# Kernel optimization log

Hardware: AMD Instinct MI355X
Metric: run time of the kernel (lower is better)

The kernel has to match this reference:

```python
import jax, jax.numpy as jnp
import numpy as np

NUM_NODES = 200000
NUM_EDGES = 600000
NUM_GRAPHS = 10000
BN_EPS = 1e-5


def setup_inputs() -> dict:
    key = jax.random.key(0)
    ks = jax.random.split(key, 10)
    x = jax.random.normal(ks[0], (NUM_NODES, 78), dtype=jnp.float32)
    edge_index = jax.random.randint(ks[1], (2, NUM_EDGES), 0, NUM_NODES, dtype=jnp.int64 if jax.config.jax_enable_x64 else jnp.int32)
    batch = jnp.sort(jax.random.randint(ks[2], (NUM_NODES,), 0, NUM_GRAPHS))
    def glorot(k, shape):
        fan_in, fan_out = shape[-2], shape[-1]
        s = jnp.sqrt(2.0 / (fan_in + fan_out))
        return jax.random.normal(k, shape, dtype=jnp.float32) * s
    return {
        "x": x,
        "edge_index": edge_index,
        "batch": batch,
        "W1_0": glorot(ks[3], (78, 128)),
        "b1_0": jnp.zeros((128,), jnp.float32),
        "W2_0": glorot(ks[4], (128, 128)),
        "b2_0": jnp.zeros((128,), jnp.float32),
        "g_0": jnp.ones((128,), jnp.float32),
        "be_0": jnp.zeros((128,), jnp.float32),
        "W1s": glorot(ks[5], (4, 128, 128)),
        "b1s": jnp.zeros((4, 128), jnp.float32),
        "W2s": glorot(ks[6], (4, 128, 128)),
        "b2s": jnp.zeros((4, 128), jnp.float32),
        "gs": jnp.ones((4, 128), jnp.float32),
        "bes": jnp.zeros((4, 128), jnp.float32),
        "fcW": glorot(ks[7], (128, 64)),
        "fcb": jnp.zeros((64,), jnp.float32),
    }


def _batchnorm(h, gamma, beta):
    # BatchNorm1d with batch statistics (training-mode normalization)
    mean = h.mean(axis=0)
    var = h.var(axis=0)  # biased, as torch uses for normalization
    return gamma * (h - mean) * jax.lax.rsqrt(var + BN_EPS) + beta


def _gin_block(h, src, dst, W1, b1, W2, b2, gamma, beta):
    # GINConv (eps=0): MLP(x + sum of neighbor messages), then ReLU + BN
    agg = jax.ops.segment_sum(h[src], dst, num_segments=NUM_NODES)  # [N, d]
    z = h + agg
    z = jax.nn.relu(z @ W1 + b1) @ W2 + b2
    z = jax.nn.relu(z)
    return _batchnorm(z, gamma, beta)


def reference(x, edge_index, batch, W1_0, b1_0, W2_0, b2_0, g_0, be_0,
              W1s, b1s, W2s, b2s, gs, bes, fcW, fcb):
    src, dst = edge_index[0], edge_index[1]
    h = _gin_block(x, src, dst, W1_0, b1_0, W2_0, b2_0, g_0, be_0)  # [N, 128]

    def body(h, params):
        W1, b1, W2, b2, g, be = params
        return _gin_block(h, src, dst, W1, b1, W2, b2, g, be), None

    h, _ = jax.lax.scan(body, h, (W1s, b1s, W2s, b2s, gs, bes))

    pooled = jax.ops.segment_sum(h, batch, num_segments=NUM_GRAPHS)  # [G, 128]
    out = jax.nn.relu(pooled @ fcW + fcb)  # [G, 64]; dropout is identity at eval
    return out
```

## Files before the change

kernel.cpp:

```cpp
#include <hip/hip_runtime.h>
#include <hip/hip_bf16.h>

#define NN 200000
#define NE 600000
#define NG 10000
#define NCH 98
#define NTILE 3125

typedef __attribute__((ext_vector_type(8))) short bfrag;
typedef __attribute__((ext_vector_type(4))) float f32x4;
typedef unsigned short u16;

static __device__ __forceinline__ u16 f2b(float x) {
  __hip_bfloat16 b = __float2bfloat16(x);
  return __builtin_bit_cast(u16, b);
}
static __device__ __forceinline__ float b2f(u16 u) {
  __hip_bfloat16 b = __builtin_bit_cast(__hip_bfloat16, u);
  return __bfloat162float(b);
}
static __device__ __forceinline__ void split(float v, u16& hi, u16& lo) {
  hi = f2b(v);
  lo = f2b(v - b2f(hi));
}

__global__ void prep_kernel(const float* __restrict__ W1_0, const float* __restrict__ W2_0,
                            const float* __restrict__ W1s, const float* __restrict__ W2s,
                            u16* __restrict__ wf) {
  int i = blockIdx.x * 256 + threadIdx.x;
  if (i >= 312 * 64) return;
  int t = i >> 6, lane = i & 63;
  const float* W;
  int KS, ct, kk, Krows, base, half;
  if (t < 24) {
    W = W1_0; KS = 3; ct = t / 3; kk = t - ct * 3; Krows = 78; base = 0; half = 12288;
  } else if (t < 56) {
    int u = t - 24;
    W = W2_0; KS = 4; ct = u >> 2; kk = u & 3; Krows = 128; base = 24576; half = 16384;
  } else {
    int u = t - 56;
    int j = u >> 6, r = u & 63;
    KS = 4; Krows = 128; half = 16384;
    if (r < 32) {
      W = W1s + j * 16384; ct = r >> 2; kk = r & 3; base = 57344 + j * 65536;
    } else {
      W = W2s + j * 16384; r -= 32; ct = r >> 2; kk = r & 3; base = 57344 + j * 65536 + 32768;
    }
  }
  int col = ct * 16 + (lane & 15);
  int idx = ((ct * KS + kk) * 64 + lane) * 8;
  for (int jj = 0; jj < 8; jj++) {
    int k = kk * 32 + 8 * (lane >> 4) + jj;
    float v = (k < Krows) ? W[k * 128 + col] : 0.f;
    u16 hi, lo;
    split(v, hi, lo);
    wf[base + idx + jj] = hi;
    wf[base + half + idx + jj] = lo;
  }
}

__global__ void hist_kernel(const int* __restrict__ dst, int* __restrict__ deg) {
  int e = blockIdx.x * 256 + threadIdx.x;
  if (e < NE) atomicAdd(&deg[dst[e]], 1);
}

__global__ void scan1_kernel(const int* __restrict__ deg, int* __restrict__ csum) {
  __shared__ int s[256];
  int base = blockIdx.x * 2048 + threadIdx.x * 8;
  int t = 0;
#pragma unroll
  for (int j = 0; j < 8; j++) {
    int idx = base + j;
    if (idx < NN) t += deg[idx];
  }
  s[threadIdx.x] = t;
  __syncthreads();
  for (int o = 128; o > 0; o >>= 1) {
    if (threadIdx.x < o) s[threadIdx.x] += s[threadIdx.x + o];
    __syncthreads();
  }
  if (threadIdx.x == 0) csum[blockIdx.x] = s[0];
}

__global__ void scan2_kernel(int* __restrict__ csum, int* __restrict__ rowptr) {
  int acc = 0;
  for (int i = 0; i < NCH; i++) {
    int v = csum[i];
    csum[i] = acc;
    acc += v;
  }
  rowptr[NN] = acc;
}

__global__ void scan3_kernel(const int* deg, const int* __restrict__ csum,
                             int* __restrict__ rowptr, int* cursor) {
  __shared__ int s[256];
  int tid = threadIdx.x;
  int base = blockIdx.x * 2048 + tid * 8;
  int loc[8];
  int t = 0;
#pragma unroll
  for (int j = 0; j < 8; j++) {
    int idx = base + j;
    int d = (idx < NN) ? deg[idx] : 0;
    loc[j] = t;
    t += d;
  }
  s[tid] = t;
  __syncthreads();
  for (int o = 1; o < 256; o <<= 1) {
    int u = (tid >= o) ? s[tid - o] : 0;
    __syncthreads();
    s[tid] += u;
    __syncthreads();
  }
  int off = csum[blockIdx.x] + s[tid] - t;
#pragma unroll
  for (int j = 0; j < 8; j++) {
    int idx = base + j;
    if (idx < NN) {
      int r = off + loc[j];
      rowptr[idx] = r;
      cursor[idx] = r;
    }
  }
}

__global__ void scatter_kernel(const int* __restrict__ src, const int* __restrict__ dst,
                               int* __restrict__ cursor, int* __restrict__ csr_src) {
  int e = blockIdx.x * 256 + threadIdx.x;
  if (e < NE) {
    int p = atomicAdd(&cursor[dst[e]], 1);
    csr_src[p] = src[e];
  }
}

template <bool FIRST>
__global__ __launch_bounds__(512, 4) void fused_kernel(
    const float* __restrict__ xin, const u16* __restrict__ hin,
    const float* __restrict__ ss,
    const int* __restrict__ rowptr, const int* __restrict__ csr_src,
    const u16* __restrict__ w1hi, const u16* __restrict__ w1lo,
    const u16* __restrict__ w2hi, const u16* __restrict__ w2lo,
    const float* __restrict__ b1, const float* __restrict__ b2,
    u16* __restrict__ hout, float* __restrict__ stats) {
  constexpr int KS1 = FIRST ? 3 : 4;
  constexpr int AH = 0, AL = 8704, TH = 17408, TL = 26112;
  __shared__ u16 lds[34816];
  const int tid = threadIdx.x;
  const int w = tid >> 6, l = tid & 63;
  const int l15 = l & 15, lg = l >> 4;
  const float bb1 = b1[w * 16 + l15];
  const float bb2 = b2[w * 16 + l15];
  float s_acc = 0.f, q_acc = 0.f;

  if (FIRST) {
    const float2* x2 = reinterpret_cast<const float2*>(xin);
    for (int tile = blockIdx.x; tile < NTILE; tile += gridDim.x) {
      const int rows0 = tile * 64;
      for (int j = 0; j < 8; j++) {
        int row = w * 8 + j;
        int node = rows0 + row;
        int beg = rowptr[node], end = rowptr[node + 1];
        int f0 = l * 2;
        if (f0 < 78) {
          size_t fv = (size_t)(f0 >> 1);
          float2 acc = x2[(size_t)node * 39 + fv];
          for (int i = beg; i < end; i += 4) {
            int last = end - 1;
            int i1 = min(i + 1, last), i2 = min(i + 2, last), i3 = min(i + 3, last);
            int s0 = csr_src[i], s1 = csr_src[i1], s2 = csr_src[i2], s3 = csr_src[i3];
            float2 v0 = x2[(size_t)s0 * 39 + fv];
            float2 v1 = x2[(size_t)s1 * 39 + fv];
            float2 v2 = x2[(size_t)s2 * 39 + fv];
            float2 v3 = x2[(size_t)s3 * 39 + fv];
            int rem = end - i;
            float m1 = rem > 1 ? 1.f : 0.f, m2 = rem > 2 ? 1.f : 0.f, m3 = rem > 3 ? 1.f : 0.f;
            acc.x += v0.x + m1 * v1.x + m2 * v2.x + m3 * v3.x;
            acc.y += v0.y + m1 * v1.y + m2 * v2.y + m3 * v3.y;
          }
          ushort2 oh, ol;
          split(acc.x, oh.x, ol.x);
          split(acc.y, oh.y, ol.y);
          *reinterpret_cast<ushort2*>(&lds[AH + row * 136 + f0]) = oh;
          *reinterpret_cast<ushort2*>(&lds[AL + row * 136 + f0]) = ol;
        } else if (f0 < 96) {
          ushort2 z = {0, 0};
          *reinterpret_cast<ushort2*>(&lds[AH + row * 136 + f0]) = z;
          *reinterpret_cast<ushort2*>(&lds[AL + row * 136 + f0]) = z;
        }
      }
      bfrag w1h[KS1], w1l[KS1];
#pragma unroll
      for (int kk = 0; kk < KS1; kk++) {
        int fi = ((w * KS1 + kk) * 64 + l) * 8;
        w1h[kk] = *reinterpret_cast<const bfrag*>(&w1hi[fi]);
        w1l[kk] = *reinterpret_cast<const bfrag*>(&w1lo[fi]);
      }
      __syncthreads();
#pragma unroll
      for (int rt = 0; rt < 4; rt++) {
        f32x4 acc = {bb1, bb1, bb1, bb1};
        const int arow = (rt * 16 + l15) * 136 + 8 * lg;
#pragma unroll
        for (int kk = 0; kk < KS1; kk++) {
          bfrag ah = *reinterpret_cast<const bfrag*>(&lds[AH + arow + kk * 32]);
          bfrag al = *reinterpret_cast<const bfrag*>(&lds[AL + arow + kk * 32]);
          acc = __builtin_amdgcn_mfma_f32_16x16x32_bf16(al, w1h[kk], acc, 0, 0, 0);
          acc = __builtin_amdgcn_mfma_f32_16x16x32_bf16(ah, w1l[kk], acc, 0, 0, 0);
          acc = __builtin_amdgcn_mfma_f32_16x16x32_bf16(ah, w1h[kk], acc, 0, 0, 0);
        }
#pragma unroll
        for (int r = 0; r < 4; r++) {
          float v = fmaxf(acc[r], 0.f);
          u16 hi, lo;
          split(v, hi, lo);
          int off = (rt * 16 + 4 * lg + r) * 136 + w * 16 + l15;
          lds[TH + off] = hi;
          lds[TL + off] = lo;
        }
      }
      bfrag w2h[4], w2l[4];
#pragma unroll
      for (int kk = 0; kk < 4; kk++) {
        int fi = ((w * 4 + kk) * 64 + l) * 8;
        w2h[kk] = *reinterpret_cast<const bfrag*>(&w2hi[fi]);
        w2l[kk] = *reinterpret_cast<const bfrag*>(&w2lo[fi]);
      }
      __syncthreads();
      u16 o16[16];
#pragma unroll
      for (int rt = 0; rt < 4; rt++) {
        f32x4 acc = {bb2, bb2, bb2, bb2};
        const int arow = (rt * 16 + l15) * 136 + 8 * lg;
#pragma unroll
        for (int kk = 0; kk < 4; kk++) {
          bfrag th = *reinterpret_cast<const bfrag*>(&lds[TH + arow + kk * 32]);
          bfrag tl = *reinterpret_cast<const bfrag*>(&lds[TL + arow + kk * 32]);
          acc = __builtin_amdgcn_mfma_f32_16x16x32_bf16(tl, w2h[kk], acc, 0, 0, 0);
          acc = __builtin_amdgcn_mfma_f32_16x16x32_bf16(th, w2l[kk], acc, 0, 0, 0);
          acc = __builtin_amdgcn_mfma_f32_16x16x32_bf16(th, w2h[kk], acc, 0, 0, 0);
        }
#pragma unroll
        for (int r = 0; r < 4; r++) {
          float v = fmaxf(acc[r], 0.f);
          s_acc += v;
          q_acc += v * v;
          o16[rt * 4 + r] = f2b(v);
        }
      }
      __syncthreads();
#pragma unroll
      for (int rt = 0; rt < 4; rt++)
#pragma unroll
        for (int r = 0; r < 4; r++)
          lds[TH + (rt * 16 + 4 * lg + r) * 136 + w * 16 + l15] = o16[rt * 4 + r];
      __syncthreads();
#pragma unroll
      for (int p2 = 0; p2 < 2; p2++) {
        int row = p2 * 32 + (tid >> 4);
        int c8 = tid & 15;
        bfrag vv = *reinterpret_cast<const bfrag*>(&lds[TH + row * 136 + c8 * 8]);
        *reinterpret_cast<bfrag*>(&hout[(size_t)(rows0 + row) * 128 + c8 * 8]) = vv;
      }
      __syncthreads();
    }
  } else {
    const bfrag* hp = reinterpret_cast<const bfrag*>(hin);
    const int k8v = l15;
    const int k8 = l15 * 8;
    float sc8[8], sh8[8];
#pragma unroll
    for (int j = 0; j < 8; j++) {
      sc8[j] = ss[k8 + j];
      sh8[j] = ss[128 + k8 + j];
    }

    int tile0 = blockIdx.x;
#pragma unroll
    for (int p = 0; p < 2; p++) {
      int row = w * 8 + p * 4 + lg;
      int node = tile0 * 64 + row;
      int beg = rowptr[node], end = rowptr[node + 1];
      float a[8];
      bfrag vs = hp[(size_t)node * 16 + k8v];
#pragma unroll
      for (int j = 0; j < 8; j++) a[j] = b2f((u16)vs[j]);
      for (int i = beg; i < end; i += 4) {
        int last = end - 1;
        int i1 = min(i + 1, last), i2 = min(i + 2, last), i3 = min(i + 3, last);
        int s0 = csr_src[i], s1 = csr_src[i1], s2 = csr_src[i2], s3 = csr_src[i3];
        bfrag v0 = hp[(size_t)s0 * 16 + k8v];
        bfrag v1 = hp[(size_t)s1 * 16 + k8v];
        bfrag v2 = hp[(size_t)s2 * 16 + k8v];
        bfrag v3 = hp[(size_t)s3 * 16 + k8v];
        int rem = end - i;
        float m1 = rem > 1 ? 1.f : 0.f, m2 = rem > 2 ? 1.f : 0.f, m3 = rem > 3 ? 1.f : 0.f;
#pragma unroll
        for (int j = 0; j < 8; j++)
          a[j] += (b2f((u16)v0[j]) + m1 * b2f((u16)v1[j])) +
                  (m2 * b2f((u16)v2[j]) + m3 * b2f((u16)v3[j]));
      }
      float cnt = (float)(end - beg + 1);
      bfrag oh, ol;
#pragma unroll
      for (int j = 0; j < 8; j++) {
        float t = a[j] * sc8[j] + cnt * sh8[j];
        u16 hi, lo;
        split(t, hi, lo);
        oh[j] = (short)hi;
        ol[j] = (short)lo;
      }
      *reinterpret_cast<bfrag*>(&lds[AH + row * 136 + k8]) = oh;
      *reinterpret_cast<bfrag*>(&lds[AL + row * 136 + k8]) = ol;
    }
    __syncthreads();

    for (int tile = tile0; tile < NTILE; tile += gridDim.x) {
      const int rows0 = tile * 64;
      int tn = tile + gridDim.x;
      bool np = tn < NTILE;
      int tnc = np ? tn : tile;

      int begN[2], endN[2];
#pragma unroll
      for (int p = 0; p < 2; p++) {
        int nodeN = tnc * 64 + w * 8 + p * 4 + lg;
        begN[p] = rowptr[nodeN];
        endN[p] = rowptr[nodeN + 1];
      }

      bfrag w1h[4], w1l[4];
#pragma unroll
      for (int kk = 0; kk < 4; kk++) {
        int fi = ((w * 4 + kk) * 64 + l) * 8;
        w1h[kk] = *reinterpret_cast<const bfrag*>(&w1hi[fi]);
        w1l[kk] = *reinterpret_cast<const bfrag*>(&w1lo[fi]);
      }
      f32x4 t1[4];
#pragma unroll
      for (int rt = 0; rt < 4; rt++) {
        f32x4 acc = {bb1, bb1, bb1, bb1};
        const int arow = (rt * 16 + l15) * 136 + 8 * lg;
#pragma unroll
        for (int kk = 0; kk < 4; kk++) {
          bfrag ah = *reinterpret_cast<const bfrag*>(&lds[AH + arow + kk * 32]);
          bfrag al = *reinterpret_cast<const bfrag*>(&lds[AL + arow + kk * 32]);
          acc = __builtin_amdgcn_mfma_f32_16x16x32_bf16(al, w1h[kk], acc, 0, 0, 0);
          acc = __builtin_amdgcn_mfma_f32_16x16x32_bf16(ah, w1l[kk], acc, 0, 0, 0);
          acc = __builtin_amdgcn_mfma_f32_16x16x32_bf16(ah, w1h[kk], acc, 0, 0, 0);
        }
        t1[rt] = acc;
      }
      __syncthreads();

      int s0[2], s1[2], s2[2], s3[2];
      float m0[2], m1[2], m2[2], m3[2], cntN[2];
#pragma unroll
      for (int p = 0; p < 2; p++) {
        int beg = begN[p], end = endN[p];
        int deg = end - beg;
        int last = end - 1;
        int i0 = beg, i1 = min(beg + 1, last), i2 = min(beg + 2, last), i3 = min(beg + 3, last);
        if (deg <= 0) { i0 = 0; i1 = 0; i2 = 0; i3 = 0; }
        s0[p] = csr_src[i0];
        s1[p] = csr_src[i1];
        s2[p] = csr_src[i2];
        s3[p] = csr_src[i3];
        m0[p] = deg > 0 ? 1.f : 0.f;
        m1[p] = deg > 1 ? 1.f : 0.f;
        m2[p] = deg > 2 ? 1.f : 0.f;
        m3[p] = deg > 3 ? 1.f : 0.f;
        cntN[p] = (float)(deg + 1);
      }

#pragma unroll
      for (int rt = 0; rt < 4; rt++) {
#pragma unroll
        for (int r = 0; r < 4; r++) {
          float v = fmaxf(t1[rt][r], 0.f);
          u16 hi, lo;
          split(v, hi, lo);
          int off = (rt * 16 + 4 * lg + r) * 136 + w * 16 + l15;
          lds[TH + off] = hi;
          lds[TL + off] = lo;
        }
      }
      bfrag w2h[4], w2l[4];
#pragma unroll
      for (int kk = 0; kk < 4; kk++) {
        int fi = ((w * 4 + kk) * 64 + l) * 8;
        w2h[kk] = *reinterpret_cast<const bfrag*>(&w2hi[fi]);
        w2l[kk] = *reinterpret_cast<const bfrag*>(&w2lo[fi]);
      }
      __syncthreads();

      bfrag selfN[2], nb0[2], nb1[2], nb2[2], nb3[2];
#pragma unroll
      for (int p = 0; p < 2; p++) {
        int nodeN = tnc * 64 + w * 8 + p * 4 + lg;
        selfN[p] = hp[(size_t)nodeN * 16 + k8v];
        nb0[p] = hp[(size_t)s0[p] * 16 + k8v];
        nb1[p] = hp[(size_t)s1[p] * 16 + k8v];
        nb2[p] = hp[(size_t)s2[p] * 16 + k8v];
        nb3[p] = hp[(size_t)s3[p] * 16 + k8v];
      }

      u16 o16[16];
#pragma unroll
      for (int rt = 0; rt < 4; rt++) {
        f32x4 acc = {bb2, bb2, bb2, bb2};
        const int arow = (rt * 16 + l15) * 136 + 8 * lg;
#pragma unroll
        for (int kk = 0; kk < 4; kk++) {
          bfrag th = *reinterpret_cast<const bfrag*>(&lds[TH + arow + kk * 32]);
          bfrag tl = *reinterpret_cast<const bfrag*>(&lds[TL + arow + kk * 32]);
          acc = __builtin_amdgcn_mfma_f32_16x16x32_bf16(tl, w2h[kk], acc, 0, 0, 0);
          acc = __builtin_amdgcn_mfma_f32_16x16x32_bf16(th, w2l[kk], acc, 0, 0, 0);
          acc = __builtin_amdgcn_mfma_f32_16x16x32_bf16(th, w2h[kk], acc, 0, 0, 0);
        }
#pragma unroll
        for (int r = 0; r < 4; r++) {
          float v = fmaxf(acc[r], 0.f);
          s_acc += v;
          q_acc += v * v;
          o16[rt * 4 + r] = f2b(v);
        }
      }
      __syncthreads();

      if (np) {
#pragma unroll
        for (int p = 0; p < 2; p++) {
          int row = w * 8 + p * 4 + lg;
          float a[8];
#pragma unroll
          for (int j = 0; j < 8; j++) a[j] = b2f((u16)selfN[p][j]);
#pragma unroll
          for (int j = 0; j < 8; j++)
            a[j] += (m0[p] * b2f((u16)nb0[p][j]) + m1[p] * b2f((u16)nb1[p][j])) +
                    (m2[p] * b2f((u16)nb2[p][j]) + m3[p] * b2f((u16)nb3[p][j]));
          int beg = begN[p], end = endN[p];
          for (int i = beg + 4; i < end; i += 4) {
            int last = end - 1;
            int i1 = min(i + 1, last), i2 = min(i + 2, last), i3 = min(i + 3, last);
            int t0 = csr_src[i], t1i = csr_src[i1], t2 = csr_src[i2], t3 = csr_src[i3];
            bfrag v0 = hp[(size_t)t0 * 16 + k8v];
            bfrag v1 = hp[(size_t)t1i * 16 + k8v];
            bfrag v2 = hp[(size_t)t2 * 16 + k8v];
            bfrag v3 = hp[(size_t)t3 * 16 + k8v];
            int rem = end - i;
            float n1 = rem > 1 ? 1.f : 0.f, n2 = rem > 2 ? 1.f : 0.f, n3 = rem > 3 ? 1.f : 0.f;
#pragma unroll
            for (int j = 0; j < 8; j++)
              a[j] += (b2f((u16)v0[j]) + n1 * b2f((u16)v1[j])) +
                      (n2 * b2f((u16)v2[j]) + n3 * b2f((u16)v3[j]));
          }
          bfrag oh, ol;
#pragma unroll
          for (int j = 0; j < 8; j++) {
            float t = a[j] * sc8[j] + cntN[p] * sh8[j];
            u16 hi, lo;
            split(t, hi, lo);
            oh[j] = (short)hi;
            ol[j] = (short)lo;
          }
          *reinterpret_cast<bfrag*>(&lds[AH + row * 136 + k8]) = oh;
          *reinterpret_cast<bfrag*>(&lds[AL + row * 136 + k8]) = ol;
        }
      }

#pragma unroll
      for (int rt = 0; rt < 4; rt++)
#pragma unroll
        for (int r = 0; r < 4; r++)
          lds[TH + (rt * 16 + 4 * lg + r) * 136 + w * 16 + l15] = o16[rt * 4 + r];
      __syncthreads();

#pragma unroll
      for (int p2 = 0; p2 < 2; p2++) {
        int row = p2 * 32 + (tid >> 4);
        int c8 = tid & 15;
        bfrag vv = *reinterpret_cast<const bfrag*>(&lds[TH + row * 136 + c8 * 8]);
        *reinterpret_cast<bfrag*>(&hout[(size_t)(rows0 + row) * 128 + c8 * 8]) = vv;
      }
    }
  }
  s_acc += __shfl_xor(s_acc, 16);
  s_acc += __shfl_xor(s_acc, 32);
  q_acc += __shfl_xor(q_acc, 16);
  q_acc += __shfl_xor(q_acc, 32);
  if (lg == 0) {
    atomicAdd(&stats[w * 16 + l15], s_acc);
    atomicAdd(&stats[128 + w * 16 + l15], q_acc);
  }
}

__global__ void bn_kernel(const float* __restrict__ stats, const float* __restrict__ gamma,
                          const float* __restrict__ beta, float* __restrict__ ss) {
  int c = threadIdx.x;
  float mean = stats[c] * (1.f / NN);
  float var = stats[128 + c] * (1.f / NN) - mean * mean;
  var = fmaxf(var, 0.f);
  float sc = gamma[c] * rsqrtf(var + 1e-5f);
  ss[c] = sc;
  ss[128 + c] = beta[c] - mean * sc;
}

__global__ void pool_kernel(const u16* __restrict__ h, const float* __restrict__ ss,
                            const int* __restrict__ batch, float* __restrict__ pooled) {
  int c = threadIdx.x;
  int n0 = blockIdx.x * 128;
  int n1 = min(n0 + 128, NN);
  float sc = ss[c], sh = ss[128 + c];
  float acc = 0.f;
  float cnt = 0.f;
  int gprev = batch[n0];
  for (int n = n0; n < n1; n++) {
    int g = batch[n];
    if (g != gprev) {
      atomicAdd(&pooled[gprev * 128 + c], sc * acc + cnt * sh);
      acc = 0.f;
      cnt = 0.f;
      gprev = g;
    }
    acc += b2f(h[(size_t)n * 128 + c]);
    cnt += 1.f;
  }
  atomicAdd(&pooled[gprev * 128 + c], sc * acc + cnt * sh);
}

__global__ void fc_kernel(const float* __restrict__ pooled, const float* __restrict__ fcW,
                          const float* __restrict__ fcb, float* __restrict__ out) {
  int i = blockIdx.x * 256 + threadIdx.x;
  if (i >= NG * 64) return;
  int g = i >> 6, o = i & 63;
  float acc = fcb[o];
#pragma unroll 8
  for (int k = 0; k < 128; k++) acc += pooled[g * 128 + k] * fcW[k * 64 + o];
  out[i] = fmaxf(acc, 0.f);
}

extern "C" void kernel_launch(void* const* d_in, const int* in_sizes, int n_in,
                              void* d_out, int out_size, void* d_ws, size_t ws_size,
                              hipStream_t stream) {
  const float* x = (const float*)d_in[0];
  const int* ei = (const int*)d_in[1];
  const int* src = ei;
  const int* dst = ei + NE;
  const int* batch = (const int*)d_in[2];
  const float* W1_0 = (const float*)d_in[3];
  const float* b1_0 = (const float*)d_in[4];
  const float* W2_0 = (const float*)d_in[5];
  const float* b2_0 = (const float*)d_in[6];
  const float* g_0 = (const float*)d_in[7];
  const float* be_0 = (const float*)d_in[8];
  const float* W1s = (const float*)d_in[9];
  const float* b1s = (const float*)d_in[10];
  const float* W2s = (const float*)d_in[11];
  const float* b2s = (const float*)d_in[12];
  const float* gs = (const float*)d_in[13];
  const float* bes = (const float*)d_in[14];
  const float* fcW = (const float*)d_in[15];
  const float* fcb = (const float*)d_in[16];

  char* ws = (char*)d_ws;
  u16* buf0 = (u16*)(ws + 0);
  u16* buf1 = (u16*)(ws + 51200000);
  float* POOLED = (float*)(ws + 102400000);
  float* STATS = (float*)(ws + 107520000);
  float* SS = (float*)(ws + 107521024);
  u16* WF = (u16*)(ws + 107522048);
  int* ROWPTR = (int*)(ws + 108161024);
  int* CURSOR = (int*)(ws + 108961040);
  int* CSRC = (int*)(ws + 109761040);
  int* CSUM = (int*)(ws + 112161040);

  prep_kernel<<<78, 256, 0, stream>>>(W1_0, W2_0, W1s, W2s, WF);

  hipMemsetAsync(CURSOR, 0, NN * 4, stream);
  hist_kernel<<<(NE + 255) / 256, 256, 0, stream>>>(dst, CURSOR);
  scan1_kernel<<<NCH, 256, 0, stream>>>(CURSOR, CSUM);
  scan2_kernel<<<1, 1, 0, stream>>>(CSUM, ROWPTR);
  scan3_kernel<<<NCH, 256, 0, stream>>>(CURSOR, CSUM, ROWPTR, CURSOR);
  scatter_kernel<<<(NE + 255) / 256, 256, 0, stream>>>(src, dst, CURSOR, CSRC);

  u16* buf[2] = {buf0, buf1};
  hipMemsetAsync(STATS, 0, 1024, stream);
  fused_kernel<true><<<512, 512, 0, stream>>>(x, nullptr, nullptr, ROWPTR, CSRC,
                                              WF, WF + 12288, WF + 24576, WF + 40960,
                                              b1_0, b2_0, buf0, STATS);
  bn_kernel<<<1, 128, 0, stream>>>(STATS, g_0, be_0, SS);

  for (int L = 1; L < 5; L++) {
    int j = L - 1;
    const u16* hin = buf[(L + 1) & 1];
    u16* hb = buf[L & 1];
    hipMemsetAsync(STATS, 0, 1024, stream);
    const u16* wl = WF + 57344 + j * 65536;
    fused_kernel<false><<<512, 512, 0, stream>>>(nullptr, hin, SS, ROWPTR, CSRC,
                                                 wl, wl + 16384, wl + 32768, wl + 49152,
                                                 b1s + j * 128, b2s + j * 128, hb, STATS);
    bn_kernel<<<1, 128, 0, stream>>>(STATS, gs + j * 128, bes + j * 128, SS);
  }

  hipMemsetAsync(POOLED, 0, (size_t)NG * 128 * 4, stream);
  pool_kernel<<<(NN + 127) / 128, 128, 0, stream>>>(buf[0], SS, batch, POOLED);
  fc_kernel<<<(NG * 64 + 255) / 256, 256, 0, stream>>>(POOLED, fcW, fcb, (float*)d_out);
}
```

Measured before the change: 740.2 us.

## Split first layer kernel and use 128-row tiles with 1024 threads for later layers

The templated fused kernel is split into a dedicated first-layer kernel and a new gin_kernel for layers 1-4. The new kernel processes 128-row tiles with 16 waves per block and reuses one LDS region for both the aggregated input and the hidden activation. It also drops the software pipelining that prefetched the next tile's neighbour gather during the MLP. The aim is more parallel gather traffic in flight per block and higher occupancy. The cost is that gather and MFMA phases no longer overlap, and 1024-thread blocks add register pressure.

After: 1.276 ms. 72.4% more time.

```diff
diff --git a/kernel.cpp b/kernel.cpp
--- a/kernel.cpp
+++ b/kernel.cpp
@@ -6,6 +6,7 @@
 #define NG 10000
 #define NCH 98
 #define NTILE 3125
+#define NT2 1563
 
 typedef __attribute__((ext_vector_type(8))) short bfrag;
 typedef __attribute__((ext_vector_type(4))) float f32x4;
@@ -135,16 +136,14 @@
   }
 }
 
-template <bool FIRST>
-__global__ __launch_bounds__(512, 4) void fused_kernel(
-    const float* __restrict__ xin, const u16* __restrict__ hin,
-    const float* __restrict__ ss,
+__global__ __launch_bounds__(512, 4) void first_kernel(
+    const float* __restrict__ xin,
     const int* __restrict__ rowptr, const int* __restrict__ csr_src,
     const u16* __restrict__ w1hi, const u16* __restrict__ w1lo,
     const u16* __restrict__ w2hi, const u16* __restrict__ w2lo,
     const float* __restrict__ b1, const float* __restrict__ b2,
     u16* __restrict__ hout, float* __restrict__ stats) {
-  constexpr int KS1 = FIRST ? 3 : 4;
+  constexpr int KS1 = 3;
   constexpr int AH = 0, AL = 8704, TH = 17408, TL = 26112;
   __shared__ u16 lds[34816];
   const int tid = threadIdx.x;
@@ -154,337 +153,115 @@
   const float bb2 = b2[w * 16 + l15];
   float s_acc = 0.f, q_acc = 0.f;
 
-  if (FIRST) {
-    const float2* x2 = reinterpret_cast<const float2*>(xin);
-    for (int tile = blockIdx.x; tile < NTILE; tile += gridDim.x) {
-      const int rows0 = tile * 64;
-      for (int j = 0; j < 8; j++) {
-        int row = w * 8 + j;
-        int node = rows0 + row;
-        int beg = rowptr[node], end = rowptr[node + 1];
-        int f0 = l * 2;
-        if (f0 < 78) {
-          size_t fv = (size_t)(f0 >> 1);
-          float2 acc = x2[(size_t)node * 39 + fv];
-          for (int i = beg; i < end; i += 4) {
-            int last = end - 1;
-            int i1 = min(i + 1, last), i2 = min(i + 2, last), i3 = min(i + 3, last);
-            int s0 = csr_src[i], s1 = csr_src[i1], s2 = csr_src[i2], s3 = csr_src[i3];
-            float2 v0 = x2[(size_t)s0 * 39 + fv];
-            float2 v1 = x2[(size_t)s1 * 39 + fv];
-            float2 v2 = x2[(size_t)s2 * 39 + fv];
-            float2 v3 = x2[(size_t)s3 * 39 + fv];
-            int rem = end - i;
-            float m1 = rem > 1 ? 1.f : 0.f, m2 = rem > 2 ? 1.f : 0.f, m3 = rem > 3 ? 1.f : 0.f;
-            acc.x += v0.x + m1 * v1.x + m2 * v2.x + m3 * v3.x;
-            acc.y += v0.y + m1 * v1.y + m2 * v2.y + m3 * v3.y;
-          }
-          ushort2 oh, ol;
-          split(acc.x, oh.x, ol.x);
-          split(acc.y, oh.y, ol.y);
-          *reinterpret_cast<ushort2*>(&lds[AH + row * 136 + f0]) = oh;
-          *reinterpret_cast<ushort2*>(&lds[AL + row * 136 + f0]) = ol;
-        } else if (f0 < 96) {
-          ushort2 z = {0, 0};
-          *reinterpret_cast<ushort2*>(&lds[AH + row * 136 + f0]) = z;
-          *reinterpret_cast<ushort2*>(&lds[AL + row * 136 + f0]) = z;
+  const float2* x2 = reinterpret_cast<const float2*>(xin);
+  for (int tile = blockIdx.x; tile < NTILE; tile += gridDim.x) {
+    const int rows0 = tile * 64;
+    for (int j = 0; j < 8; j++) {
+      int row = w * 8 + j;
+      int node = rows0 + row;
+      int beg = rowptr[node], end = rowptr[node + 1];
+      int f0 = l * 2;
+      if (f0 < 78) {
+        size_t fv = (size_t)(f0 >> 1);
+        float2 acc = x2[(size_t)node * 39 + fv];
+        for (int i = beg; i < end; i += 4) {
+          int last = end - 1;
+          int i1 = min(i + 1, last), i2 = min(i + 2, last), i3 = min(i + 3, last);
+          int s0 = csr_src[i], s1 = csr_src[i1], s2 = csr_src[i2], s3 = csr_src[i3];
+          float2 v0 = x2[(size_t)s0 * 39 + fv];
+          float2 v1 = x2[(size_t)s1 * 39 + fv];
+          float2 v2 = x2[(size_t)s2 * 39 + fv];
+          float2 v3 = x2[(size_t)s3 * 39 + fv];
+          int rem = end - i;
+          float m1 = rem > 1 ? 1.f : 0.f, m2 = rem > 2 ? 1.f : 0.f, m3 = rem > 3 ? 1.f : 0.f;
+          acc.x += v0.x + m1 * v1.x + m2 * v2.x + m3 * v3.x;
+          acc.y += v0.y + m1 * v1.y + m2 * v2.y + m3 * v3.y;
         }
-      }
-      bfrag w1h[KS1], w1l[KS1];
+        ushort2 oh, ol;
+        split(acc.x, oh.x, ol.x);
+        split(acc.y, oh.y, ol.y);
+        *reinterpret_cast<ushort2*>(&lds[AH + row * 136 + f0]) = oh;
+        *reinterpret_cast<ushort2*>(&lds[AL + row * 136 + f0]) = ol;
+      } else if (f0 < 96) {
+        ushort2 z = {0, 0};
+        *reinterpret_cast<ushort2*>(&lds[AH + row * 136 + f0]) = z;
+        *reinterpret_cast<ushort2*>(&lds[AL + row * 136 + f0]) = z;
+      }
+    }
+    bfrag w1h[KS1], w1l[KS1];
+#pragma unroll
+    for (int kk = 0; kk < KS1; kk++) {
+      int fi = ((w * KS1 + kk) * 64 + l) * 8;
+      w1h[kk] = *reinterpret_cast<const bfrag*>(&w1hi[fi]);
+      w1l[kk] = *reinterpret_cast<const bfrag*>(&w1lo[fi]);
+    }
+    __syncthreads();
+#pragma unroll
+    for (int rt = 0; rt < 4; rt++) {
+      f32x4 acc = {bb1, bb1, bb1, bb1};
+      const int arow = (rt * 16 + l15) * 136 + 8 * lg;
 #pragma unroll
       for (int kk = 0; kk < KS1; kk++) {
-        int fi = ((w * KS1 + kk) * 64 + l) * 8;
-        w1h[kk] = *reinterpret_cast<const bfrag*>(&w1hi[fi]);
-        w1l[kk] = *reinterpret_cast<const bfrag*>(&w1lo[fi]);
-      }
-      __syncthreads();
-#pragma unroll
-      for (int rt = 0; rt < 4; rt++) {
-        f32x4 acc = {bb1, bb1, bb1, bb1};
-        const int arow = (rt * 16 + l15) * 136 + 8 * lg;
-#pragma unroll
-        for (int kk = 0; kk < KS1; kk++) {
-          bfrag ah = *reinterpret_cast<const bfrag*>(&lds[AH + arow + kk * 32]);
-          bfrag al = *reinterpret_cast<const bfrag*>(&lds[AL + arow + kk * 32]);
-          acc = __builtin_amdgcn_mfma_f32_16x16x32_bf16(al, w1h[kk], acc, 0, 0, 0);
-          acc = __builtin_amdgcn_mfma_f32_16x16x32_bf16(ah, w1l[kk], acc, 0, 0, 0);
-          acc = __builtin_amdgcn_mfma_f32_16x16x32_bf16(ah, w1h[kk], acc, 0, 0, 0);
-        }
-#pragma unroll
-        for (int r = 0; r < 4; r++) {
-          float v = fmaxf(acc[r], 0.f);
-          u16 hi, lo;
-          split(v, hi, lo);
-          int off = (rt * 16 + 4 * lg + r) * 136 + w * 16 + l15;
-          lds[TH + off] = hi;
-          lds[TL + off] = lo;
-        }
-      }
-      bfrag w2h[4], w2l[4];
+        bfrag ah = *reinterpret_cast<const bfrag*>(&lds[AH + arow + kk * 32]);
+        bfrag al = *reinterpret_cast<const bfrag*>(&lds[AL + arow + kk * 32]);
+        acc = __builtin_amdgcn_mfma_f32_16x16x32_bf16(al, w1h[kk], acc, 0, 0, 0);
+        acc = __builtin_amdgcn_mfma_f32_16x16x32_bf16(ah, w1l[kk], acc, 0, 0, 0);
+        acc = __builtin_amdgcn_mfma_f32_16x16x32_bf16(ah, w1h[kk], acc, 0, 0, 0);
+      }
+#pragma unroll
+      for (int r = 0; r < 4; r++) {
+        float v = fmaxf(acc[r], 0.f);
+        u16 hi, lo;
+        split(v, hi, lo);
+        int off = (rt * 16 + 4 * lg + r) * 136 + w * 16 + l15;
+        lds[TH + off] = hi;
+        lds[TL + off] = lo;
+      }
+    }
+    bfrag w2h[4], w2l[4];
+#pragma unroll
+    for (int kk = 0; kk < 4; kk++) {
+      int fi = ((w * 4 + kk) * 64 + l) * 8;
+      w2h[kk] = *reinterpret_cast<const bfrag*>(&w2hi[fi]);
+      w2l[kk] = *reinterpret_cast<const bfrag*>(&w2lo[fi]);
+    }
+    __syncthreads();
+    u16 o16[16];
+#pragma unroll
+    for (int rt = 0; rt < 4; rt++) {
+      f32x4 acc = {bb2, bb2, bb2, bb2};
+      const int arow = (rt * 16 + l15) * 136 + 8 * lg;
 #pragma unroll
       for (int kk = 0; kk < 4; kk++) {
-        int fi = ((w * 4 + kk) * 64 + l) * 8;
-        w2h[kk] = *reinterpret_cast<const bfrag*>(&w2hi[fi]);
-        w2l[kk] = *reinterpret_cast<const bfrag*>(&w2lo[fi]);
-      }
-      __syncthreads();
-      u16 o16[16];
-#pragma unroll
-      for (int rt = 0; rt < 4; rt++) {
-        f32x4 acc = {bb2, bb2, bb2, bb2};
-        const int arow = (rt * 16 + l15) * 136 + 8 * lg;
-#pragma unroll
-        for (int kk = 0; kk < 4; kk++) {
-          bfrag th = *reinterpret_cast<const bfrag*>(&lds[TH + arow + kk * 32]);
-          bfrag tl = *reinterpret_cast<const bfrag*>(&lds[TL + arow + kk * 32]);
-          acc = __builtin_amdgcn_mfma_f32_16x16x32_bf16(tl, w2h[kk], acc, 0, 0, 0);
-          acc = __builtin_amdgcn_mfma_f32_16x16x32_bf16(th, w2l[kk], acc, 0, 0, 0);
-          acc = __builtin_amdgcn_mfma_f32_16x16x32_bf16(th, w2h[kk], acc, 0, 0, 0);
-        }
-#pragma unroll
-        for (int r = 0; r < 4; r++) {
-          float v = fmaxf(acc[r], 0.f);
-          s_acc += v;
-          q_acc += v * v;
-          o16[rt * 4 + r] = f2b(v);
-        }
-      }
-      __syncthreads();
-#pragma unroll
-      for (int rt = 0; rt < 4; rt++)
-#pragma unroll
-        for (int r = 0; r < 4; r++)
-          lds[TH + (rt * 16 + 4 * lg + r) * 136 + w * 16 + l15] = o16[rt * 4 + r];
-      __syncthreads();
-#pragma unroll
-      for (int p2 = 0; p2 < 2; p2++) {
-        int row = p2 * 32 + (tid >> 4);
-        int c8 = tid & 15;
-        bfrag vv = *reinterpret_cast<const bfrag*>(&lds[TH + row * 136 + c8 * 8]);
-        *reinterpret_cast<bfrag*>(&hout[(size_t)(rows0 + row) * 128 + c8 * 8]) = vv;
-      }
-      __syncthreads();
-    }
-  } else {
-    const bfrag* hp = reinterpret_cast<const bfrag*>(hin);
-    const int k8v = l15;
-    const int k8 = l15 * 8;
-    float sc8[8], sh8[8];
-#pragma unroll
-    for (int j = 0; j < 8; j++) {
-      sc8[j] = ss[k8 + j];
-      sh8[j] = ss[128 + k8 + j];
-    }
-
-    int tile0 = blockIdx.x;
-#pragma unroll
-    for (int p = 0; p < 2; p++) {
-      int row = w * 8 + p * 4 + lg;
-      int node = tile0 * 64 + row;
-      int beg = rowptr[node], end = rowptr[node + 1];
-      float a[8];
-      bfrag vs = hp[(size_t)node * 16 + k8v];
-#pragma unroll
-      for (int j = 0; j < 8; j++) a[j] = b2f((u16)vs[j]);
-      for (int i = beg; i < end; i += 4) {
-        int last = end - 1;
-        int i1 = min(i + 1, last), i2 = min(i + 2, last), i3 = min(i + 3, last);
-        int s0 = csr_src[i], s1 = csr_src[i1], s2 = csr_src[i2], s3 = csr_src[i3];
-        bfrag v0 = hp[(size_t)s0 * 16 + k8v];
-        bfrag v1 = hp[(size_t)s1 * 16 + k8v];
-        bfrag v2 = hp[(size_t)s2 * 16 + k8v];
-        bfrag v3 = hp[(size_t)s3 * 16 + k8v];
-        int rem = end - i;
-        float m1 = rem > 1 ? 1.f : 0.f, m2 = rem > 2 ? 1.f : 0.f, m3 = rem > 3 ? 1.f : 0.f;
-#pragma unroll
-        for (int j = 0; j < 8; j++)
-          a[j] += (b2f((u16)v0[j]) + m1 * b2f((u16)v1[j])) +
-                  (m2 * b2f((u16)v2[j]) + m3 * b2f((u16)v3[j]));
-      }
-      float cnt = (float)(end - beg + 1);
-      bfrag oh, ol;
-#pragma unroll
-      for (int j = 0; j < 8; j++) {
-        float t = a[j] * sc8[j] + cnt * sh8[j];
-        u16 hi, lo;
-        split(t, hi, lo);
-        oh[j] = (short)hi;
-        ol[j] = (short)lo;
-      }
-      *reinterpret_cast<bfrag*>(&lds[AH + row * 136 + k8]) = oh;
-      *reinterpret_cast<bfrag*>(&lds[AL + row * 136 + k8]) = ol;
-    }
-    __syncthreads();
-
-    for (int tile = tile0; tile < NTILE; tile += gridDim.x) {
-      const int rows0 = tile * 64;
-      int tn = tile + gridDim.x;
-      bool np = tn < NTILE;
-      int tnc = np ? tn : tile;
-
-      int begN[2], endN[2];
-#pragma unroll
-      for (int p = 0; p < 2; p++) {
-        int nodeN = tnc * 64 + w * 8 + p * 4 + lg;
-        begN[p] = rowptr[nodeN];
-        endN[p] = rowptr[nodeN + 1];
-      }
-
-      bfrag w1h[4], w1l[4];
-#pragma unroll
-      for (int kk = 0; kk < 4; kk++) {
-        int fi = ((w * 4 + kk) * 64 + l) * 8;
-        w1h[kk] = *reinterpret_cast<const bfrag*>(&w1hi[fi]);
-        w1l[kk] = *reinterpret_cast<const bfrag*>(&w1lo[fi]);
-      }
-      f32x4 t1[4];
-#pragma unroll
-      for (int rt = 0; rt < 4; rt++) {
-        f32x4 acc = {bb1, bb1, bb1, bb1};
-        const int arow = (rt * 16 + l15) * 136 + 8 * lg;
-#pragma unroll
-        for (int kk = 0; kk < 4; kk++) {
-          bfrag ah = *reinterpret_cast<const bfrag*>(&lds[AH + arow + kk * 32]);
-          bfrag al = *reinterpret_cast<const bfrag*>(&lds[AL + arow + kk * 32]);
-          acc = __builtin_amdgcn_mfma_f32_16x16x32_bf16(al, w1h[kk], acc, 0, 0, 0);
-          acc = __builtin_amdgcn_mfma_f32_16x16x32_bf16(ah, w1l[kk], acc, 0, 0, 0);
-          acc = __builtin_amdgcn_mfma_f32_16x16x32_bf16(ah, w1h[kk], acc, 0, 0, 0);
-        }
-        t1[rt] = acc;
-      }
-      __syncthreads();
-
-      int s0[2], s1[2], s2[2], s3[2];
-      float m0[2], m1[2], m2[2], m3[2], cntN[2];
-#pragma unroll
-      for (int p = 0; p < 2; p++) {
-        int beg = begN[p], end = endN[p];
-        int deg = end - beg;
-        int last = end - 1;
-        int i0 = beg, i1 = min(beg + 1, last), i2 = min(beg + 2, last), i3 = min(beg + 3, last);
-        if (deg <= 0) { i0 = 0; i1 = 0; i2 = 0; i3 = 0; }
-        s0[p] = csr_src[i0];
-        s1[p] = csr_src[i1];
-        s2[p] = csr_src[i2];
-        s3[p] = csr_src[i3];
-        m0[p] = deg > 0 ? 1.f : 0.f;
-        m1[p] = deg > 1 ? 1.f : 0.f;
-        m2[p] = deg > 2 ? 1.f : 0.f;
-        m3[p] = deg > 3 ? 1.f : 0.f;
-        cntN[p] = (float)(deg + 1);
-      }
-
-#pragma unroll
-      for (int rt = 0; rt < 4; rt++) {
-#pragma unroll
-        for (int r = 0; r < 4; r++) {
-          float v = fmaxf(t1[rt][r], 0.f);
-          u16 hi, lo;
-          split(v, hi, lo);
-          int off = (rt * 16 + 4 * lg + r) * 136 + w * 16 + l15;
-          lds[TH + off] = hi;
-          lds[TL + off] = lo;
-        }
-      }
-      bfrag w2h[4], w2l[4];
-#pragma unroll
-      for (int kk = 0; kk < 4; kk++) {
-        int fi = ((w * 4 + kk) * 64 + l) * 8;
-        w2h[kk] = *reinterpret_cast<const bfrag*>(&w2hi[fi]);
-        w2l[kk] = *reinterpret_cast<const bfrag*>(&w2lo[fi]);
-      }
-      __syncthreads();
-
-      bfrag selfN[2], nb0[2], nb1[2], nb2[2], nb3[2];
-#pragma unroll
-      for (int p = 0; p < 2; p++) {
-        int nodeN = tnc * 64 + w * 8 + p * 4 + lg;
-        selfN[p] = hp[(size_t)nodeN * 16 + k8v];
-        nb0[p] = hp[(size_t)s0[p] * 16 + k8v];
-        nb1[p] = hp[(size_t)s1[p] * 16 + k8v];
-        nb2[p] = hp[(size_t)s2[p] * 16 + k8v];
-        nb3[p] = hp[(size_t)s3[p] * 16 + k8v];
-      }
-
-      u16 o16[16];
-#pragma unroll
-      for (int rt = 0; rt < 4; rt++) {
-        f32x4 acc = {bb2, bb2, bb2, bb2};
-        const int arow = (rt * 16 + l15) * 136 + 8 * lg;
-#pragma unroll
-        for (int kk = 0; kk < 4; kk++) {
-          bfrag th = *reinterpret_cast<const bfrag*>(&lds[TH + arow + kk * 32]);
-          bfrag tl = *reinterpret_cast<const bfrag*>(&lds[TL + arow + kk * 32]);
-          acc = __builtin_amdgcn_mfma_f32_16x16x32_bf16(tl, w2h[kk], acc, 0, 0, 0);
-          acc = __builtin_amdgcn_mfma_f32_16x16x32_bf16(th, w2l[kk], acc, 0, 0, 0);
-          acc = __builtin_amdgcn_mfma_f32_16x16x32_bf16(th, w2h[kk], acc, 0, 0, 0);
-        }
-#pragma unroll
-        for (int r = 0; r < 4; r++) {
-          float v = fmaxf(acc[r], 0.f);
-          s_acc += v;
-          q_acc += v * v;
-          o16[rt * 4 + r] = f2b(v);
-        }
-      }
-      __syncthreads();
-
-      if (np) {
-#pragma unroll
-        for (int p = 0; p < 2; p++) {
-          int row = w * 8 + p * 4 + lg;
-          float a[8];
-#pragma unroll
-          for (int j = 0; j < 8; j++) a[j] = b2f((u16)selfN[p][j]);
-#pragma unroll
-          for (int j = 0; j < 8; j++)
-            a[j] += (m0[p] * b2f((u16)nb0[p][j]) + m1[p] * b2f((u16)nb1[p][j])) +
-                    (m2[p] * b2f((u16)nb2[p][j]) + m3[p] * b2f((u16)nb3[p][j]));
-          int beg = begN[p], end = endN[p];
-          for (int i = beg + 4; i < end; i += 4) {
-            int last = end - 1;
-            int i1 = min(i + 1, last), i2 = min(i + 2, last), i3 = min(i + 3, last);
-            int t0 = csr_src[i], t1i = csr_src[i1], t2 = csr_src[i2], t3 = csr_src[i3];
-            bfrag v0 = hp[(size_t)t0 * 16 + k8v];
-            bfrag v1 = hp[(size_t)t1i * 16 + k8v];
-            bfrag v2 = hp[(size_t)t2 * 16 + k8v];
-            bfrag v3 = hp[(size_t)t3 * 16 + k8v];
-            int rem = end - i;
-            float n1 = rem > 1 ? 1.f : 0.f, n2 = rem > 2 ? 1.f : 0.f, n3 = rem > 3 ? 1.f : 0.f;
-#pragma unroll
-            for (int j = 0; j < 8; j++)
-              a[j] += (b2f((u16)v0[j]) + n1 * b2f((u16)v1[j])) +
-                      (n2 * b2f((u16)v2[j]) + n3 * b2f((u16)v3[j]));
-          }
-          bfrag oh, ol;
-#pragma unroll
-          for (int j = 0; j < 8; j++) {
-            float t = a[j] * sc8[j] + cntN[p] * sh8[j];
-            u16 hi, lo;
-            split(t, hi, lo);
-            oh[j] = (short)hi;
-            ol[j] = (short)lo;
-          }
-          *reinterpret_cast<bfrag*>(&lds[AH + row * 136 + k8]) = oh;
-          *reinterpret_cast<bfrag*>(&lds[AL + row * 136 + k8]) = ol;
-        }
-      }
-
-#pragma unroll
-      for (int rt = 0; rt < 4; rt++)
-#pragma unroll
-        for (int r = 0; r < 4; r++)
-          lds[TH + (rt * 16 + 4 * lg + r) * 136 + w * 16 + l15] = o16[rt * 4 + r];
-      __syncthreads();
-
-#pragma unroll
-      for (int p2 = 0; p2 < 2; p2++) {
-        int row = p2 * 32 + (tid >> 4);
-        int c8 = tid & 15;
-        bfrag vv = *reinterpret_cast<const bfrag*>(&lds[TH + row * 136 + c8 * 8]);
-        *reinterpret_cast<bfrag*>(&hout[(size_t)(rows0 + row) * 128 + c8 * 8]) = vv;
-      }
-    }
+        bfrag th = *reinterpret_cast<const bfrag*>(&lds[TH + arow + kk * 32]);
+        bfrag tl = *reinterpret_cast<const bfrag*>(&lds[TL + arow + kk * 32]);
+        acc = __builtin_amdgcn_mfma_f32_16x16x32_bf16(tl, w2h[kk], acc, 0, 0, 0);
+        acc = __builtin_amdgcn_mfma_f32_16x16x32_bf16(th, w2l[kk], acc, 0, 0, 0);
+        acc = __builtin_amdgcn_mfma_f32_16x16x32_bf16(th, w2h[kk], acc, 0, 0, 0);
+      }
+#pragma unroll
+      for (int r = 0; r < 4; r++) {
+        float v = fmaxf(acc[r], 0.f);
+        s_acc += v;
+        q_acc += v * v;
+        o16[rt * 4 + r] = f2b(v);
+      }
+    }
+    __syncthreads();
+#pragma unroll
+    for (int rt = 0; rt < 4; rt++)
+#pragma unroll
+      for (int r = 0; r < 4; r++)
+        lds[TH + (rt * 16 + 4 * lg + r) * 136 + w * 16 + l15] = o16[rt * 4 + r];
+    __syncthreads();
+#pragma unroll
+    for (int p2 = 0; p2 < 2; p2++) {
+      int row = p2 * 32 + (tid >> 4);
+      int c8 = tid & 15;
+      bfrag vv = *reinterpret_cast<const bfrag*>(&lds[TH + row * 136 + c8 * 8]);
+      *reinterpret_cast<bfrag*>(&hout[(size_t)(rows0 + row) * 128 + c8 * 8]) = vv;
+    }
+    __syncthreads();
   }
   s_acc += __shfl_xor(s_acc, 16);
   s_acc += __shfl_xor(s_acc, 32);
@@ -493,6 +270,179 @@
   if (lg == 0) {
     atomicAdd(&stats[w * 16 + l15], s_acc);
     atomicAdd(&stats[128 + w * 16 + l15], q_acc);
+  }
+}
+
+__global__ __launch_bounds__(1024, 8) void gin_kernel(
+    const u16* __restrict__ hin, const float* __restrict__ ss,
+    const int* __restrict__ rowptr, const int* __restrict__ csr_src,
+    const u16* __restrict__ w1hi, const u16* __restrict__ w1lo,
+    const u16* __restrict__ w2hi, const u16* __restrict__ w2lo,
+    const float* __restrict__ b1, const float* __restrict__ b2,
+    u16* __restrict__ hout, float* __restrict__ stats) {
+  constexpr int AH = 0, AL = 17408;
+  __shared__ u16 lds[34816];
+  const int tid = threadIdx.x;
+  const int w = tid >> 6, l = tid & 63;
+  const int l15 = l & 15, lg = l >> 4;
+  const int ct = w & 7;
+  const int hrow = (w >> 3) * 64;
+  const float bb1 = b1[ct * 16 + l15];
+  const float bb2 = b2[ct * 16 + l15];
+  const bfrag* hp = reinterpret_cast<const bfrag*>(hin);
+  const int k8v = l15;
+  const int k8 = l15 * 8;
+  float sc8[8], sh8[8];
+#pragma unroll
+  for (int j = 0; j < 8; j++) {
+    sc8[j] = ss[k8 + j];
+    sh8[j] = ss[128 + k8 + j];
+  }
+  float s_acc = 0.f, q_acc = 0.f;
+
+  for (int tile = blockIdx.x; tile < NT2; tile += gridDim.x) {
+    const int rows0 = tile * 128;
+
+    for (int p = 0; p < 2; p++) {
+      int row = w * 8 + p * 4 + lg;
+      int node = rows0 + row;
+      bfrag oh, ol;
+      if (node < NN) {
+        int beg = rowptr[node], end = rowptr[node + 1];
+        float a[8];
+        bfrag vs = hp[(size_t)node * 16 + k8v];
+#pragma unroll
+        for (int j = 0; j < 8; j++) a[j] = b2f((u16)vs[j]);
+        for (int i = beg; i < end; i += 4) {
+          int last = end - 1;
+          int i1 = min(i + 1, last), i2 = min(i + 2, last), i3 = min(i + 3, last);
+          int s0 = csr_src[i], s1 = csr_src[i1], s2 = csr_src[i2], s3 = csr_src[i3];
+          bfrag v0 = hp[(size_t)s0 * 16 + k8v];
+          bfrag v1 = hp[(size_t)s1 * 16 + k8v];
+          bfrag v2 = hp[(size_t)s2 * 16 + k8v];
+          bfrag v3 = hp[(size_t)s3 * 16 + k8v];
+          int rem = end - i;
+          float m1 = rem > 1 ? 1.f : 0.f, m2 = rem > 2 ? 1.f : 0.f, m3 = rem > 3 ? 1.f : 0.f;
+#pragma unroll
+          for (int j = 0; j < 8; j++)
+            a[j] += (b2f((u16)v0[j]) + m1 * b2f((u16)v1[j])) +
+                    (m2 * b2f((u16)v2[j]) + m3 * b2f((u16)v3[j]));
+        }
+        float cnt = (float)(end - beg + 1);
+#pragma unroll
+        for (int j = 0; j < 8; j++) {
+          float t = a[j] * sc8[j] + cnt * sh8[j];
+          u16 hi, lo;
+          split(t, hi, lo);
+          oh[j] = (short)hi;
+          ol[j] = (short)lo;
+        }
+      } else {
+#pragma unroll
+        for (int j = 0; j < 8; j++) { oh[j] = 0; ol[j] = 0; }
+      }
+      *reinterpret_cast<bfrag*>(&lds[AH + row * 136 + k8]) = oh;
+      *reinterpret_cast<bfrag*>(&lds[AL + row * 136 + k8]) = ol;
+    }
+    bfrag w1h[4], w1l[4];
+#pragma unroll
+    for (int kk = 0; kk < 4; kk++) {
+      int fi = ((ct * 4 + kk) * 64 + l) * 8;
+      w1h[kk] = *reinterpret_cast<const bfrag*>(&w1hi[fi]);
+      w1l[kk] = *reinterpret_cast<const bfrag*>(&w1lo[fi]);
+    }
+    __syncthreads();
+
+    f32x4 t1[4];
+#pragma unroll
+    for (int rt = 0; rt < 4; rt++) {
+      f32x4 acc = {bb1, bb1, bb1, bb1};
+      const int arow = (hrow + rt * 16 + l15) * 136 + 8 * lg;
+#pragma unroll
+      for (int kk = 0; kk < 4; kk++) {
+        bfrag ah = *reinterpret_cast<const bfrag*>(&lds[AH + arow + kk * 32]);
+        bfrag al = *reinterpret_cast<const bfrag*>(&lds[AL + arow + kk * 32]);
+        acc = __builtin_amdgcn_mfma_f32_16x16x32_bf16(al, w1h[kk], acc, 0, 0, 0);
+        acc = __builtin_amdgcn_mfma_f32_16x16x32_bf16(ah, w1l[kk], acc, 0, 0, 0);
+        acc = __builtin_amdgcn_mfma_f32_16x16x32_bf16(ah, w1h[kk], acc, 0, 0, 0);
+      }
+      t1[rt] = acc;
+    }
+    __syncthreads();
+
+#pragma unroll
+    for (int rt = 0; rt < 4; rt++) {
+#pragma unroll
+      for (int r = 0; r < 4; r++) {
+        float v = fmaxf(t1[rt][r], 0.f);
+        u16 hi, lo;
+        split(v, hi, lo);
+        int off = (hrow + rt * 16 + 4 * lg + r) * 136 + ct * 16 + l15;
+        lds[AH + off] = hi;
+        lds[AL + off] = lo;
+      }
+    }
+    bfrag w2h[4], w2l[4];
+#pragma unroll
+    for (int kk = 0; kk < 4; kk++) {
+      int fi = ((ct * 4 + kk) * 64 + l) * 8;
+      w2h[kk] = *reinterpret_cast<const bfrag*>(&w2hi[fi]);
+      w2l[kk] = *reinterpret_cast<const bfrag*>(&w2lo[fi]);
+    }
+    __syncthreads();
+
+    u16 o16[16];
+#pragma unroll
+    for (int rt = 0; rt < 4; rt++) {
+      f32x4 acc = {bb2, bb2, bb2, bb2};
+      const int arow = (hrow + rt * 16 + l15) * 136 + 8 * lg;
+#pragma unroll
+      for (int kk = 0; kk < 4; kk++) {
+        bfrag th = *reinterpret_cast<const bfrag*>(&lds[AH + arow + kk * 32]);
+        bfrag tl = *reinterpret_cast<const bfrag*>(&lds[AL + arow + kk * 32]);
+        acc = __builtin_amdgcn_mfma_f32_16x16x32_bf16(tl, w2h[kk], acc, 0, 0, 0);
+        acc = __builtin_amdgcn_mfma_f32_16x16x32_bf16(th, w2l[kk], acc, 0, 0, 0);
+        acc = __builtin_amdgcn_mfma_f32_16x16x32_bf16(th, w2h[kk], acc, 0, 0, 0);
+      }
+#pragma unroll
+      for (int r = 0; r < 4; r++) {
+        float v = fmaxf(acc[r], 0.f);
+        int gr = rows0 + hrow + rt * 16 + 4 * lg + r;
+        if (gr < NN) {
+          s_acc += v;
+          q_acc += v * v;
+        }
+        o16[rt * 4 + r] = f2b(v);
+      }
+    }
+    __syncthreads();
+
+#pragma unroll
+    for (int rt = 0; rt < 4; rt++)
+#pragma unroll
+      for (int r = 0; r < 4; r++)
+        lds[AH + (hrow + rt * 16 + 4 * lg + r) * 136 + ct * 16 + l15] = o16[rt * 4 + r];
+    __syncthreads();
+
+#pragma unroll
+    for (int p2 = 0; p2 < 2; p2++) {
+      int row = p2 * 64 + (tid >> 4);
+      int c8 = tid & 15;
+      int gr = rows0 + row;
+      if (gr < NN) {
+        bfrag vv = *reinterpret_cast<const bfrag*>(&lds[AH + row * 136 + c8 * 8]);
+        *reinterpret_cast<bfrag*>(&hout[(size_t)gr * 128 + c8 * 8]) = vv;
+      }
+    }
+    __syncthreads();
+  }
+  s_acc += __shfl_xor(s_acc, 16);
+  s_acc += __shfl_xor(s_acc, 32);
+  q_acc += __shfl_xor(q_acc, 16);
+  q_acc += __shfl_xor(q_acc, 32);
+  if (lg == 0) {
+    atomicAdd(&stats[ct * 16 + l15], s_acc);
+    atomicAdd(&stats[128 + ct * 16 + l15], q_acc);
   }
 }
 
@@ -587,9 +537,9 @@
 
   u16* buf[2] = {buf0, buf1};
   hipMemsetAsync(STATS, 0, 1024, stream);
-  fused_kernel<true><<<512, 512, 0, stream>>>(x, nullptr, nullptr, ROWPTR, CSRC,
-                                              WF, WF + 12288, WF + 24576, WF + 40960,
-                                              b1_0, b2_0, buf0, STATS);
+  first_kernel<<<512, 512, 0, stream>>>(x, ROWPTR, CSRC,
+                                        WF, WF + 12288, WF + 24576, WF + 40960,
+                                        b1_0, b2_0, buf0, STATS);
   bn_kernel<<<1, 128, 0, stream>>>(STATS, g_0, be_0, SS);
 
   for (int L = 1; L < 5; L++) {
@@ -598,9 +548,9 @@
     u16* hb = buf[L & 1];
     hipMemsetAsync(STATS, 0, 1024, stream);
     const u16* wl = WF + 57344 + j * 65536;
-    fused_kernel<false><<<512, 512, 0, stream>>>(nullptr, hin, SS, ROWPTR, CSRC,
-                                                 wl, wl + 16384, wl + 32768, wl + 49152,
-                                                 b1s + j * 128, b2s + j * 128, hb, STATS);
+    gin_kernel<<<512, 1024, 0, stream>>>(hin, SS, ROWPTR, CSRC,
+                                         wl, wl + 16384, wl + 32768, wl + 49152,
+                                         b1s + j * 128, b2s + j * 128, hb, STATS);
     bn_kernel<<<1, 128, 0, stream>>>(STATS, gs + j * 128, bes + j * 128, SS);
   }
 
```
